# Kernel optimization log

Measured on AMD Instinct MI355X. Metric: run time of the kernel, lower is better.

The kernel has to match this reference:

```python
import jax, jax.numpy as jnp
import numpy as np


def setup_inputs() -> dict:
    key = jax.random.key(0)
    k1, k2, *kw = jax.random.split(key, 12)
    N, E = 10000, 320000
    D_IN, D_HID, D_EMB, D_PRED = 2, 128, 256, 128

    def lin(k, fan_in, fan_out):
        bound = 1.0 / np.sqrt(fan_in)
        kw_, kb_ = jax.random.split(k)
        W = jax.random.uniform(kw_, (fan_in, fan_out), jnp.float32, -bound, bound)
        b = jax.random.uniform(kb_, (fan_out,), jnp.float32, -bound, bound)
        return W, b

    W1, b1 = lin(kw[0], D_IN, D_HID)
    W2, b2 = lin(kw[1], D_HID, D_EMB)
    Wp1, bp1 = lin(kw[2], D_EMB, D_PRED)
    Wp2, bp2 = lin(kw[3], D_PRED, 1)

    src = jax.random.randint(k1, (E,), 0, N, dtype=jnp.int32)
    dst = jax.random.randint(k2, (E,), 0, N, dtype=jnp.int32)
    return {
        "W1": W1, "b1": b1, "W2": W2, "b2": b2,
        "Wp1": Wp1, "bp1": bp1, "Wp2": Wp2, "bp2": bp2,
        "src": src, "dst": dst, "num_nodes": N,
    }


def reference(W1, b1, W2, b2, Wp1, bp1, Wp2, bp2, src, dst, num_nodes):
    N = num_nodes
    E = src.shape[0]
    ones = jnp.ones((E,), jnp.float32)
    # node features = [in_degree, out_degree]  -> [N, 2]
    in_deg = jax.ops.segment_sum(ones, dst, num_segments=N)
    out_deg = jax.ops.segment_sum(ones, src, num_segments=N)
    x = jnp.stack([in_deg, out_deg], axis=1)

    def gcn_agg(h):
        # sum of messages from source nodes into destination nodes (SpMM-like)
        return jax.ops.segment_sum(h[src], dst, num_segments=N)

    h = jax.nn.relu(gcn_agg(x) @ W1 + b1)        # [N, 128]
    h = gcn_agg(h) @ W2 + b2                     # [N, 256]
    h = jax.nn.relu(h)
    graph_embedding = jnp.sum(h, axis=0)         # [256] (dgl.sum_nodes, single graph)
    m = jax.nn.relu(graph_embedding @ Wp1 + bp1)
    metric = m @ Wp2 + bp2                       # [1]
    return (graph_embedding, metric)
```

## Files before the change

kernel.cpp:

```cpp
#include <hip/hip_runtime.h>

#define N_NODES 10000
#define CAPLOG 7
#define CAP 128
#define NPART 16
#define NBH 128
#define TBH 512

__global__ __launch_bounds__(TBH) void hist_kernel(const int* __restrict__ src,
                                                   const int* __restrict__ dst,
                                                   unsigned int* __restrict__ cnt, int E) {
  __shared__ unsigned int hist[N_NODES];
  const int tid = threadIdx.x, bid = blockIdx.x;
  for (int i = tid; i < N_NODES; i += TBH) hist[i] = 0;
  __syncthreads();
  const int chunk = (E + NBH - 1) / NBH;
  const int e0 = bid * chunk, e1 = min(E, e0 + chunk);
  for (int e = e0 + tid; e < e1; e += TBH) {
    atomicAdd(&hist[dst[e]], 1u);
    atomicAdd(&hist[src[e]], 0x10000u);
  }
  __syncthreads();
  unsigned int* outb = cnt + (size_t)bid * N_NODES;
  for (int i = tid; i < N_NODES; i += TBH) outb[i] = hist[i];
}

__global__ __launch_bounds__(256) void scan_kernel(const unsigned int* __restrict__ cnt,
                                                   unsigned int* __restrict__ off,
                                                   unsigned int* __restrict__ pack) {
  const int n = blockIdx.x * 256 + threadIdx.x;
  if (n >= N_NODES) return;
  unsigned run_in = 0, run_out = 0;
  for (int b = 0; b < NBH; ++b) {
    unsigned v = cnt[(size_t)b * N_NODES + n];
    off[(size_t)b * N_NODES + n] = run_in;
    run_in += v & 0xFFFFu;
    run_out += v >> 16;
  }
  pack[n] = run_in | (run_out << 16);
}

__global__ __launch_bounds__(TBH) void scatter_kernel(const int* __restrict__ src,
                                                      const int* __restrict__ dst,
                                                      const unsigned int* __restrict__ off,
                                                      unsigned short* __restrict__ slots,
                                                      int E) {
  __shared__ unsigned int cur[N_NODES];
  const int tid = threadIdx.x, bid = blockIdx.x;
  const unsigned int* ob = off + (size_t)bid * N_NODES;
  for (int i = tid; i < N_NODES; i += TBH) cur[i] = ob[i];
  __syncthreads();
  const int chunk = (E + NBH - 1) / NBH;
  const int e0 = bid * chunk, e1 = min(E, e0 + chunk);
  for (int e = e0 + tid; e < e1; e += TBH) {
    int d = dst[e];
    unsigned idx = atomicAdd(&cur[d], 1u);
    if (idx < CAP) slots[(d << CAPLOG) + idx] = (unsigned short)src[e];
  }
}

__global__ __launch_bounds__(256) void agg1_kernel(const unsigned int* __restrict__ pack,
                                                   const unsigned short* __restrict__ slots,
                                                   float2* __restrict__ a) {
  const int tid = threadIdx.x;
  const int hw = tid >> 5, hl = tid & 31;
  const int node = blockIdx.x * 8 + hw;
  const int deg = min((int)(pack[node] & 0xFFFFu), CAP);
  const int base = node << CAPLOG;
  float a0 = 0.f, a1 = 0.f;
  for (int e = hl; e < deg; e += 32) {
    unsigned v = pack[slots[base + e]];
    a0 += (float)(v & 0xFFFFu);
    a1 += (float)(v >> 16);
  }
#pragma unroll
  for (int off = 16; off > 0; off >>= 1) {
    a0 += __shfl_xor(a0, off);
    a1 += __shfl_xor(a1, off);
  }
  if (hl == 0) a[node] = make_float2(a0, a1);
}

__global__ __launch_bounds__(256) void agg2gemm2_kernel(const unsigned int* __restrict__ pack,
                                                        const unsigned short* __restrict__ slots,
                                                        const float2* __restrict__ a,
                                                        const float* __restrict__ W1,
                                                        const float* __restrict__ b1,
                                                        const float* __restrict__ W2,
                                                        const float* __restrict__ b2,
                                                        float* __restrict__ ge_p) {
  __shared__ float s_tile[8][128];
  const int tid = threadIdx.x, bid = blockIdx.x;
  const int hw = tid >> 5, hl = tid & 31;

  float w10[4], w11[4], bb[4];
#pragma unroll
  for (int c = 0; c < 4; ++c) {
    w10[c] = W1[4 * hl + c];
    w11[c] = W1[128 + 4 * hl + c];
    bb[c] = b1[4 * hl + c];
  }
  const int node = bid * 8 + hw;
  const int deg = min((int)(pack[node] & 0xFFFFu), CAP);
  float acc0 = 0.f, acc1 = 0.f, acc2 = 0.f, acc3 = 0.f;
  int rem = deg, eb = node << CAPLOG;
  while (rem > 0) {
    int cnt = min(rem, 32);
    float va0 = 0.f, va1 = 0.f;
    if (hl < cnt) {
      float2 av = a[slots[eb + hl]];
      va0 = av.x;
      va1 = av.y;
    }
    for (int j = 0; j < cnt; ++j) {
      float x0 = __shfl(va0, j, 32);
      float x1 = __shfl(va1, j, 32);
      acc0 += fmaxf(fmaf(x0, w10[0], fmaf(x1, w11[0], bb[0])), 0.f);
      acc1 += fmaxf(fmaf(x0, w10[1], fmaf(x1, w11[1], bb[1])), 0.f);
      acc2 += fmaxf(fmaf(x0, w10[2], fmaf(x1, w11[2], bb[2])), 0.f);
      acc3 += fmaxf(fmaf(x0, w10[3], fmaf(x1, w11[3], bb[3])), 0.f);
    }
    rem -= cnt;
    eb += cnt;
  }
  s_tile[hw][4 * hl + 0] = acc0;
  s_tile[hw][4 * hl + 1] = acc1;
  s_tile[hw][4 * hl + 2] = acc2;
  s_tile[hw][4 * hl + 3] = acc3;
  __syncthreads();

  float d[8];
#pragma unroll
  for (int n = 0; n < 8; ++n) d[n] = 0.f;
#pragma unroll
  for (int kc = 0; kc < 4; ++kc) {
    float wv[32];
#pragma unroll
    for (int c = 0; c < 32; ++c) wv[c] = W2[(kc * 32 + c) * 256 + tid];
#pragma unroll
    for (int n = 0; n < 8; ++n) {
      const float4* row4 = (const float4*)&s_tile[n][kc * 32];
      float t0 = 0.f, t1 = 0.f, t2 = 0.f, t3 = 0.f;
#pragma unroll
      for (int q = 0; q < 8; ++q) {
        float4 rv = row4[q];
        t0 = fmaf(rv.x, wv[4 * q + 0], t0);
        t1 = fmaf(rv.y, wv[4 * q + 1], t1);
        t2 = fmaf(rv.z, wv[4 * q + 2], t2);
        t3 = fmaf(rv.w, wv[4 * q + 3], t3);
      }
      d[n] += (t0 + t1) + (t2 + t3);
    }
  }

  const float bj = b2[tid];
  float accge = 0.f;
#pragma unroll
  for (int n = 0; n < 8; ++n) accge += fmaxf(d[n] + bj, 0.f);
  atomicAdd(&ge_p[((bid & (NPART - 1)) << 8) + tid], accge);
}

__global__ __launch_bounds__(256) void head_kernel(const float* __restrict__ ge_p,
                                                   const float* __restrict__ Wp1,
                                                   const float* __restrict__ bp1,
                                                   const float* __restrict__ Wp2,
                                                   const float* __restrict__ bp2,
                                                   float* __restrict__ out) {
  __shared__ float s_ge[256];
  __shared__ float s_m[256];
  int tid = threadIdx.x;
  float g = 0.f;
#pragma unroll
  for (int p = 0; p < NPART; ++p) g += ge_p[p * 256 + tid];
  s_ge[tid] = g;
  out[tid] = g;
  __syncthreads();
  int j = tid & 127, halfk = tid >> 7;
  float d = halfk ? 0.f : bp1[j];
  int k0 = halfk << 7;
#pragma unroll 8
  for (int k = k0; k < k0 + 128; ++k) d = fmaf(s_ge[k], Wp1[k * 128 + j], d);
  s_m[tid] = d;
  __syncthreads();
  if (tid < 128) s_m[tid] = fmaxf(s_m[tid] + s_m[tid + 128], 0.f) * Wp2[tid];
  __syncthreads();
  if (tid < 64) {
    float v = s_m[tid] + s_m[tid + 64];
#pragma unroll
    for (int off = 32; off > 0; off >>= 1) v += __shfl_xor(v, off);
    if (tid == 0) out[256] = v + bp2[0];
  }
}

extern "C" void kernel_launch(void* const* d_in, const int* in_sizes, int n_in,
                              void* d_out, int out_size, void* d_ws, size_t ws_size,
                              hipStream_t stream) {
  const float* W1 = (const float*)d_in[0];
  const float* b1 = (const float*)d_in[1];
  const float* W2 = (const float*)d_in[2];
  const float* b2 = (const float*)d_in[3];
  const float* Wp1 = (const float*)d_in[4];
  const float* bp1 = (const float*)d_in[5];
  const float* Wp2 = (const float*)d_in[6];
  const float* bp2 = (const float*)d_in[7];
  const int* src = (const int*)d_in[8];
  const int* dst = (const int*)d_in[9];
  const int E = in_sizes[8];
  const int N = N_NODES;

  char* p = (char*)d_ws;
  float* ge_p = (float*)p;               p += (size_t)NPART * 256 * 4;
  unsigned int* pack = (unsigned int*)p; p += (size_t)N * 4;
  unsigned short* slots = (unsigned short*)p; p += (size_t)N * CAP * 2;
  float2* a = (float2*)p;                p += (size_t)N * 8;
  unsigned int* cnt = (unsigned int*)p;  p += (size_t)NBH * N * 4;
  unsigned int* off = (unsigned int*)p;
  float* out = (float*)d_out;

  hipMemsetAsync(d_ws, 0, (size_t)NPART * 256 * 4, stream);

  hist_kernel<<<NBH, TBH, 0, stream>>>(src, dst, cnt, E);
  scan_kernel<<<(N + 255) / 256, 256, 0, stream>>>(cnt, off, pack);
  scatter_kernel<<<NBH, TBH, 0, stream>>>(src, dst, off, slots, E);
  agg1_kernel<<<N / 8, 256, 0, stream>>>(pack, slots, a);
  agg2gemm2_kernel<<<N / 8, 256, 0, stream>>>(pack, slots, a, W1, b1, W2, b2, ge_p);
  head_kernel<<<1, 256, 0, stream>>>(ge_p, Wp1, bp1, Wp2, bp2, out);
}
```

Before: 135.0 us.

## Replace histogram-scan-scatter CSR build with per-node-range full-edge scan and fuse head

Replaces the three-kernel histogram, scan and scatter CSR construction with a prep kernel that packs src/dst into 32-bit edge words, followed by a build kernel. In the build kernel, each block scans every edge and keeps only those whose destination or source falls in its 40-node range. The first aggregation now stores packed integer degree sums instead of float2, halving the gather traffic. The head MLP is fused into the last block of the GEMM kernel through a done counter, and the memset is folded into the prep kernel. The cost is that each of the 250 blocks rereads the whole edge list, trading redundant L2 reads for fewer launches and no large count and offset arrays. Slot order within a node becomes nondeterministic, which changes float summation order.

```diff
diff --git a/kernel.cpp b/kernel.cpp
--- a/kernel.cpp
+++ b/kernel.cpp
@@ -4,92 +4,120 @@
 #define CAPLOG 7
 #define CAP 128
 #define NPART 16
-#define NBH 128
-#define TBH 512
-
-__global__ __launch_bounds__(TBH) void hist_kernel(const int* __restrict__ src,
-                                                   const int* __restrict__ dst,
-                                                   unsigned int* __restrict__ cnt, int E) {
-  __shared__ unsigned int hist[N_NODES];
-  const int tid = threadIdx.x, bid = blockIdx.x;
-  for (int i = tid; i < N_NODES; i += TBH) hist[i] = 0;
-  __syncthreads();
-  const int chunk = (E + NBH - 1) / NBH;
-  const int e0 = bid * chunk, e1 = min(E, e0 + chunk);
-  for (int e = e0 + tid; e < e1; e += TBH) {
-    atomicAdd(&hist[dst[e]], 1u);
-    atomicAdd(&hist[src[e]], 0x10000u);
-  }
-  __syncthreads();
-  unsigned int* outb = cnt + (size_t)bid * N_NODES;
-  for (int i = tid; i < N_NODES; i += TBH) outb[i] = hist[i];
-}
-
-__global__ __launch_bounds__(256) void scan_kernel(const unsigned int* __restrict__ cnt,
-                                                   unsigned int* __restrict__ off,
-                                                   unsigned int* __restrict__ pack) {
-  const int n = blockIdx.x * 256 + threadIdx.x;
-  if (n >= N_NODES) return;
-  unsigned run_in = 0, run_out = 0;
-  for (int b = 0; b < NBH; ++b) {
-    unsigned v = cnt[(size_t)b * N_NODES + n];
-    off[(size_t)b * N_NODES + n] = run_in;
-    run_in += v & 0xFFFFu;
-    run_out += v >> 16;
-  }
-  pack[n] = run_in | (run_out << 16);
-}
-
-__global__ __launch_bounds__(TBH) void scatter_kernel(const int* __restrict__ src,
+
+#define NBB 250
+#define TBB 1024
+#define NPB 40
+
+#define PREP_T 256
+__global__ __launch_bounds__(PREP_T) void prep_kernel(const int* __restrict__ src,
                                                       const int* __restrict__ dst,
-                                                      const unsigned int* __restrict__ off,
-                                                      unsigned short* __restrict__ slots,
+                                                      unsigned int* __restrict__ ed,
+                                                      float* __restrict__ ge_p,
+                                                      unsigned int* __restrict__ done,
                                                       int E) {
-  __shared__ unsigned int cur[N_NODES];
-  const int tid = threadIdx.x, bid = blockIdx.x;
-  const unsigned int* ob = off + (size_t)bid * N_NODES;
-  for (int i = tid; i < N_NODES; i += TBH) cur[i] = ob[i];
-  __syncthreads();
-  const int chunk = (E + NBH - 1) / NBH;
-  const int e0 = bid * chunk, e1 = min(E, e0 + chunk);
-  for (int e = e0 + tid; e < e1; e += TBH) {
-    int d = dst[e];
-    unsigned idx = atomicAdd(&cur[d], 1u);
-    if (idx < CAP) slots[(d << CAPLOG) + idx] = (unsigned short)src[e];
-  }
+  const int t = blockIdx.x * PREP_T + threadIdx.x;
+  if (t < NPART * 256) ge_p[t] = 0.f;
+  if (t == NPART * 256) *done = 0u;
+  const int nv = E >> 3;
+  if (t < nv) {
+    const int4* s4 = (const int4*)src;
+    const int4* d4 = (const int4*)dst;
+    int4 s0 = s4[2 * t], s1 = s4[2 * t + 1];
+    int4 d0 = d4[2 * t], d1 = d4[2 * t + 1];
+    uint4 o0, o1;
+    o0.x = (unsigned)d0.x | ((unsigned)s0.x << 16);
+    o0.y = (unsigned)d0.y | ((unsigned)s0.y << 16);
+    o0.z = (unsigned)d0.z | ((unsigned)s0.z << 16);
+    o0.w = (unsigned)d0.w | ((unsigned)s0.w << 16);
+    o1.x = (unsigned)d1.x | ((unsigned)s1.x << 16);
+    o1.y = (unsigned)d1.y | ((unsigned)s1.y << 16);
+    o1.z = (unsigned)d1.z | ((unsigned)s1.z << 16);
+    o1.w = (unsigned)d1.w | ((unsigned)s1.w << 16);
+    ((uint4*)ed)[2 * t + 0] = o0;
+    ((uint4*)ed)[2 * t + 1] = o1;
+  }
+  if (t == 0) {
+    for (int e = E & ~7; e < E; ++e)
+      ed[e] = ((unsigned)dst[e] & 0xFFFFu) | ((unsigned)src[e] << 16);
+  }
+}
+
+__global__ __launch_bounds__(TBB) void build_kernel(const unsigned int* __restrict__ ed,
+                                                    unsigned short* __restrict__ slots,
+                                                    unsigned int* __restrict__ pack,
+                                                    int E) {
+  __shared__ unsigned int cin[NPB], cout[NPB];
+  const int tid = threadIdx.x;
+  const unsigned n0 = blockIdx.x * NPB;
+  if (tid < NPB) { cin[tid] = 0u; cout[tid] = 0u; }
+  __syncthreads();
+  const int nv = E >> 2;
+  const uint4* e4 = (const uint4*)ed;
+  for (int c = tid; c < nv; c += TBB) {
+    uint4 v = e4[c];
+    unsigned w[4] = {v.x, v.y, v.z, v.w};
+#pragma unroll
+    for (int q = 0; q < 4; ++q) {
+      const unsigned d = w[q] & 0xFFFFu, s = w[q] >> 16;
+      const unsigned rd = d - n0;
+      if (rd < NPB) {
+        unsigned idx = atomicAdd(&cin[rd], 1u);
+        if (idx < CAP) slots[(d << CAPLOG) + idx] = (unsigned short)s;
+      }
+      const unsigned rs = s - n0;
+      if (rs < NPB) atomicAdd(&cout[rs], 1u);
+    }
+  }
+  if (tid == 0) {
+    for (int e = E & ~3; e < E; ++e) {
+      const unsigned d = ed[e] & 0xFFFFu, s = ed[e] >> 16;
+      const unsigned rd = d - n0;
+      if (rd < NPB) {
+        unsigned idx = atomicAdd(&cin[rd], 1u);
+        if (idx < CAP) slots[(d << CAPLOG) + idx] = (unsigned short)s;
+      }
+      const unsigned rs = s - n0;
+      if (rs < NPB) atomicAdd(&cout[rs], 1u);
+    }
+  }
+  __syncthreads();
+  if (tid < NPB) pack[n0 + tid] = cin[tid] | (cout[tid] << 16);
 }
 
 __global__ __launch_bounds__(256) void agg1_kernel(const unsigned int* __restrict__ pack,
                                                    const unsigned short* __restrict__ slots,
-                                                   float2* __restrict__ a) {
+                                                   unsigned int* __restrict__ a) {
   const int tid = threadIdx.x;
   const int hw = tid >> 5, hl = tid & 31;
   const int node = blockIdx.x * 8 + hw;
   const int deg = min((int)(pack[node] & 0xFFFFu), CAP);
   const int base = node << CAPLOG;
-  float a0 = 0.f, a1 = 0.f;
-  for (int e = hl; e < deg; e += 32) {
-    unsigned v = pack[slots[base + e]];
-    a0 += (float)(v & 0xFFFFu);
-    a1 += (float)(v >> 16);
-  }
-#pragma unroll
-  for (int off = 16; off > 0; off >>= 1) {
-    a0 += __shfl_xor(a0, off);
-    a1 += __shfl_xor(a1, off);
-  }
-  if (hl == 0) a[node] = make_float2(a0, a1);
+  unsigned acc = 0u;
+  for (int e = hl; e < deg; e += 32) acc += pack[slots[base + e]];
+#pragma unroll
+  for (int off = 16; off > 0; off >>= 1) acc += (unsigned)__shfl_xor((int)acc, off);
+  if (hl == 0) a[node] = acc;
 }
 
 __global__ __launch_bounds__(256) void agg2gemm2_kernel(const unsigned int* __restrict__ pack,
                                                         const unsigned short* __restrict__ slots,
-                                                        const float2* __restrict__ a,
+                                                        const unsigned int* __restrict__ a,
                                                         const float* __restrict__ W1,
                                                         const float* __restrict__ b1,
                                                         const float* __restrict__ W2,
                                                         const float* __restrict__ b2,
-                                                        float* __restrict__ ge_p) {
+                                                        const float* __restrict__ Wp1,
+                                                        const float* __restrict__ bp1,
+                                                        const float* __restrict__ Wp2,
+                                                        const float* __restrict__ bp2,
+                                                        float* __restrict__ ge_p,
+                                                        unsigned int* __restrict__ done,
+                                                        float* __restrict__ out) {
   __shared__ float s_tile[8][128];
+  __shared__ float s_ge[256];
+  __shared__ float s_m[256];
+  __shared__ int s_last;
   const int tid = threadIdx.x, bid = blockIdx.x;
   const int hw = tid >> 5, hl = tid & 31;
 
@@ -106,15 +134,12 @@
   int rem = deg, eb = node << CAPLOG;
   while (rem > 0) {
     int cnt = min(rem, 32);
-    float va0 = 0.f, va1 = 0.f;
-    if (hl < cnt) {
-      float2 av = a[slots[eb + hl]];
-      va0 = av.x;
-      va1 = av.y;
-    }
+    unsigned av = 0u;
+    if (hl < cnt) av = a[slots[eb + hl]];
     for (int j = 0; j < cnt; ++j) {
-      float x0 = __shfl(va0, j, 32);
-      float x1 = __shfl(va1, j, 32);
+      const unsigned v = (unsigned)__shfl((int)av, j, 32);
+      const float x0 = (float)(v & 0xFFFFu);
+      const float x1 = (float)(v >> 16);
       acc0 += fmaxf(fmaf(x0, w10[0], fmaf(x1, w11[0], bb[0])), 0.f);
       acc1 += fmaxf(fmaf(x0, w10[1], fmaf(x1, w11[1], bb[1])), 0.f);
       acc2 += fmaxf(fmaf(x0, w10[2], fmaf(x1, w11[2], bb[2])), 0.f);
@@ -158,29 +183,28 @@
 #pragma unroll
   for (int n = 0; n < 8; ++n) accge += fmaxf(d[n] + bj, 0.f);
   atomicAdd(&ge_p[((bid & (NPART - 1)) << 8) + tid], accge);
-}
-
-__global__ __launch_bounds__(256) void head_kernel(const float* __restrict__ ge_p,
-                                                   const float* __restrict__ Wp1,
-                                                   const float* __restrict__ bp1,
-                                                   const float* __restrict__ Wp2,
-                                                   const float* __restrict__ bp2,
-                                                   float* __restrict__ out) {
-  __shared__ float s_ge[256];
-  __shared__ float s_m[256];
-  int tid = threadIdx.x;
+
+  __syncthreads();
+  if (tid == 0) {
+    __threadfence();
+    s_last = (atomicAdd(done, 1u) == (unsigned)(gridDim.x - 1)) ? 1 : 0;
+  }
+  __syncthreads();
+  if (!s_last) return;
+
   float g = 0.f;
 #pragma unroll
-  for (int p = 0; p < NPART; ++p) g += ge_p[p * 256 + tid];
+  for (int p = 0; p < NPART; ++p)
+    g += __hip_atomic_load(&ge_p[p * 256 + tid], __ATOMIC_RELAXED, __HIP_MEMORY_SCOPE_AGENT);
   s_ge[tid] = g;
   out[tid] = g;
   __syncthreads();
-  int j = tid & 127, halfk = tid >> 7;
-  float d = halfk ? 0.f : bp1[j];
-  int k0 = halfk << 7;
+  const int j = tid & 127, halfk = tid >> 7;
+  float dd = halfk ? 0.f : bp1[j];
+  const int k0 = halfk << 7;
 #pragma unroll 8
-  for (int k = k0; k < k0 + 128; ++k) d = fmaf(s_ge[k], Wp1[k * 128 + j], d);
-  s_m[tid] = d;
+  for (int k = k0; k < k0 + 128; ++k) dd = fmaf(s_ge[k], Wp1[k * 128 + j], dd);
+  s_m[tid] = dd;
   __syncthreads();
   if (tid < 128) s_m[tid] = fmaxf(s_m[tid] + s_m[tid + 128], 0.f) * Wp2[tid];
   __syncthreads();
@@ -210,19 +234,18 @@
 
   char* p = (char*)d_ws;
   float* ge_p = (float*)p;               p += (size_t)NPART * 256 * 4;
+  unsigned int* done = (unsigned int*)p; p += 16;
   unsigned int* pack = (unsigned int*)p; p += (size_t)N * 4;
+  unsigned int* a = (unsigned int*)p;    p += (size_t)N * 4;
   unsigned short* slots = (unsigned short*)p; p += (size_t)N * CAP * 2;
-  float2* a = (float2*)p;                p += (size_t)N * 8;
-  unsigned int* cnt = (unsigned int*)p;  p += (size_t)NBH * N * 4;
-  unsigned int* off = (unsigned int*)p;
+  unsigned int* ed = (unsigned int*)p;
   float* out = (float*)d_out;
 
-  hipMemsetAsync(d_ws, 0, (size_t)NPART * 256 * 4, stream);
-
-  hist_kernel<<<NBH, TBH, 0, stream>>>(src, dst, cnt, E);
-  scan_kernel<<<(N + 255) / 256, 256, 0, stream>>>(cnt, off, pack);
-  scatter_kernel<<<NBH, TBH, 0, stream>>>(src, dst, off, slots, E);
+  const int nv8 = (E + 7) / 8;
+  const int prep_threads = (nv8 > NPART * 256 + 1) ? nv8 : (NPART * 256 + 1);
+  prep_kernel<<<(prep_threads + PREP_T - 1) / PREP_T, PREP_T, 0, stream>>>(src, dst, ed, ge_p, done, E);
+  build_kernel<<<NBB, TBB, 0, stream>>>(ed, slots, pack, E);
   agg1_kernel<<<N / 8, 256, 0, stream>>>(pack, slots, a);
-  agg2gemm2_kernel<<<N / 8, 256, 0, stream>>>(pack, slots, a, W1, b1, W2, b2, ge_p);
-  head_kernel<<<1, 256, 0, stream>>>(ge_p, Wp1, bp1, Wp2, bp2, out);
-}
+  agg2gemm2_kernel<<<N / 8, 256, 0, stream>>>(pack, slots, a, W1, b1, W2, b2,
+                                              Wp1, bp1, Wp2, bp2, ge_p, done, out);
+}
```

Result: slower. 166.0 us (+23.0%).

## Materialize layer-1 activations, gather rows in agg2, fuse head via last-block

Applied to the files above, without the earlier changes.

Moves the first linear+ReLU into agg1, which now writes a full [N,128] hidden matrix. agg2 then gathers and sums neighbor rows with wide loads instead of recomputing relu(W1·x) per edge through shuffles. The memset and head kernel launches are removed: hist zeroes the partial sums and a done counter, and the last block of agg2 computes the head after a threadfence and atomic ticket. The scan also sums the packed in/out counts as one word. In exchange, agg2 does more gather traffic (about 5 MB of h written and reread per edge), and the packed 16-bit in/out counters become fragile if a node's degree carries past 16 bits.

```diff
diff --git a/kernel.cpp b/kernel.cpp
--- a/kernel.cpp
+++ b/kernel.cpp
@@ -9,10 +9,15 @@
 
 __global__ __launch_bounds__(TBH) void hist_kernel(const int* __restrict__ src,
                                                    const int* __restrict__ dst,
-                                                   unsigned int* __restrict__ cnt, int E) {
+                                                   unsigned int* __restrict__ cnt,
+                                                   float* __restrict__ ge_p,
+                                                   unsigned int* __restrict__ done,
+                                                   int E) {
   __shared__ unsigned int hist[N_NODES];
   const int tid = threadIdx.x, bid = blockIdx.x;
   for (int i = tid; i < N_NODES; i += TBH) hist[i] = 0;
+  if (bid < NPART && tid < 256) ge_p[(bid << 8) + tid] = 0.f;
+  if (bid == NPART && tid == 0) *done = 0u;
   __syncthreads();
   const int chunk = (E + NBH - 1) / NBH;
   const int e0 = bid * chunk, e1 = min(E, e0 + chunk);
@@ -30,14 +35,14 @@
                                                    unsigned int* __restrict__ pack) {
   const int n = blockIdx.x * 256 + threadIdx.x;
   if (n >= N_NODES) return;
-  unsigned run_in = 0, run_out = 0;
+  unsigned run = 0;
+#pragma unroll 8
   for (int b = 0; b < NBH; ++b) {
     unsigned v = cnt[(size_t)b * N_NODES + n];
-    off[(size_t)b * N_NODES + n] = run_in;
-    run_in += v & 0xFFFFu;
-    run_out += v >> 16;
-  }
-  pack[n] = run_in | (run_out << 16);
+    off[(size_t)b * N_NODES + n] = run;
+    run += v;
+  }
+  pack[n] = run;
 }
 
 __global__ __launch_bounds__(TBH) void scatter_kernel(const int* __restrict__ src,
@@ -54,79 +59,77 @@
   const int e0 = bid * chunk, e1 = min(E, e0 + chunk);
   for (int e = e0 + tid; e < e1; e += TBH) {
     int d = dst[e];
-    unsigned idx = atomicAdd(&cur[d], 1u);
+    unsigned idx = atomicAdd(&cur[d], 1u) & 0xFFFFu;
     if (idx < CAP) slots[(d << CAPLOG) + idx] = (unsigned short)src[e];
   }
 }
 
-__global__ __launch_bounds__(256) void agg1_kernel(const unsigned int* __restrict__ pack,
-                                                   const unsigned short* __restrict__ slots,
-                                                   float2* __restrict__ a) {
+__global__ __launch_bounds__(256) void agg1h_kernel(const unsigned int* __restrict__ pack,
+                                                    const unsigned short* __restrict__ slots,
+                                                    const float* __restrict__ W1,
+                                                    const float* __restrict__ b1,
+                                                    float* __restrict__ h) {
   const int tid = threadIdx.x;
   const int hw = tid >> 5, hl = tid & 31;
   const int node = blockIdx.x * 8 + hw;
   const int deg = min((int)(pack[node] & 0xFFFFu), CAP);
   const int base = node << CAPLOG;
-  float a0 = 0.f, a1 = 0.f;
-  for (int e = hl; e < deg; e += 32) {
-    unsigned v = pack[slots[base + e]];
-    a0 += (float)(v & 0xFFFFu);
-    a1 += (float)(v >> 16);
-  }
-#pragma unroll
-  for (int off = 16; off > 0; off >>= 1) {
-    a0 += __shfl_xor(a0, off);
-    a1 += __shfl_xor(a1, off);
-  }
-  if (hl == 0) a[node] = make_float2(a0, a1);
+  unsigned acc = 0u;
+  for (int e = hl; e < deg; e += 32) acc += pack[slots[base + e]];
+#pragma unroll
+  for (int off = 16; off > 0; off >>= 1) acc += (unsigned)__shfl_xor((int)acc, off, 32);
+  const float a0 = (float)(acc & 0xFFFFu);
+  const float a1 = (float)(acc >> 16);
+  const int c = 4 * hl;
+  float4 hv;
+  hv.x = fmaxf(fmaf(a0, W1[c + 0], fmaf(a1, W1[128 + c + 0], b1[c + 0])), 0.f);
+  hv.y = fmaxf(fmaf(a0, W1[c + 1], fmaf(a1, W1[128 + c + 1], b1[c + 1])), 0.f);
+  hv.z = fmaxf(fmaf(a0, W1[c + 2], fmaf(a1, W1[128 + c + 2], b1[c + 2])), 0.f);
+  hv.w = fmaxf(fmaf(a0, W1[c + 3], fmaf(a1, W1[128 + c + 3], b1[c + 3])), 0.f);
+  ((float4*)h)[node * 32 + hl] = hv;
 }
 
 __global__ __launch_bounds__(256) void agg2gemm2_kernel(const unsigned int* __restrict__ pack,
                                                         const unsigned short* __restrict__ slots,
-                                                        const float2* __restrict__ a,
-                                                        const float* __restrict__ W1,
-                                                        const float* __restrict__ b1,
+                                                        const float* __restrict__ h,
                                                         const float* __restrict__ W2,
                                                         const float* __restrict__ b2,
-                                                        float* __restrict__ ge_p) {
+                                                        const float* __restrict__ Wp1,
+                                                        const float* __restrict__ bp1,
+                                                        const float* __restrict__ Wp2,
+                                                        const float* __restrict__ bp2,
+                                                        float* __restrict__ ge_p,
+                                                        unsigned int* __restrict__ done,
+                                                        float* __restrict__ out) {
   __shared__ float s_tile[8][128];
+  __shared__ float s_ge[256];
+  __shared__ float s_m[256];
+  __shared__ int s_last;
   const int tid = threadIdx.x, bid = blockIdx.x;
-  const int hw = tid >> 5, hl = tid & 31;
-
-  float w10[4], w11[4], bb[4];
-#pragma unroll
-  for (int c = 0; c < 4; ++c) {
-    w10[c] = W1[4 * hl + c];
-    w11[c] = W1[128 + 4 * hl + c];
-    bb[c] = b1[4 * hl + c];
-  }
-  const int node = bid * 8 + hw;
-  const int deg = min((int)(pack[node] & 0xFFFFu), CAP);
-  float acc0 = 0.f, acc1 = 0.f, acc2 = 0.f, acc3 = 0.f;
-  int rem = deg, eb = node << CAPLOG;
-  while (rem > 0) {
-    int cnt = min(rem, 32);
-    float va0 = 0.f, va1 = 0.f;
-    if (hl < cnt) {
-      float2 av = a[slots[eb + hl]];
-      va0 = av.x;
-      va1 = av.y;
+  const int wv = tid >> 6, lane = tid & 63;
+  const float2* h2 = (const float2*)h;
+
+#pragma unroll
+  for (int nn = 0; nn < 2; ++nn) {
+    const int node = bid * 8 + 2 * wv + nn;
+    const int deg = min((int)(pack[node] & 0xFFFFu), CAP);
+    const unsigned* sl32 = (const unsigned*)(slots + (node << CAPLOG));
+    float2 acc = make_float2(0.f, 0.f);
+    for (int i0 = 0; i0 < deg; i0 += 8) {
+      const uint4 sw = ((const uint4*)sl32)[i0 >> 3];
+      const unsigned ss[4] = {sw.x, sw.y, sw.z, sw.w};
+#pragma unroll
+      for (int q = 0; q < 8; ++q) {
+        if (i0 + q < deg) {
+          const int s = (q & 1) ? (int)(ss[q >> 1] >> 16) : (int)(ss[q >> 1] & 0xFFFFu);
+          const float2 v = h2[s * 64 + lane];
+          acc.x += v.x;
+          acc.y += v.y;
+        }
+      }
     }
-    for (int j = 0; j < cnt; ++j) {
-      float x0 = __shfl(va0, j, 32);
-      float x1 = __shfl(va1, j, 32);
-      acc0 += fmaxf(fmaf(x0, w10[0], fmaf(x1, w11[0], bb[0])), 0.f);
-      acc1 += fmaxf(fmaf(x0, w10[1], fmaf(x1, w11[1], bb[1])), 0.f);
-      acc2 += fmaxf(fmaf(x0, w10[2], fmaf(x1, w11[2], bb[2])), 0.f);
-      acc3 += fmaxf(fmaf(x0, w10[3], fmaf(x1, w11[3], bb[3])), 0.f);
-    }
-    rem -= cnt;
-    eb += cnt;
-  }
-  s_tile[hw][4 * hl + 0] = acc0;
-  s_tile[hw][4 * hl + 1] = acc1;
-  s_tile[hw][4 * hl + 2] = acc2;
-  s_tile[hw][4 * hl + 3] = acc3;
+    ((float2*)&s_tile[2 * wv + nn][0])[lane] = acc;
+  }
   __syncthreads();
 
   float d[8];
@@ -134,9 +137,9 @@
   for (int n = 0; n < 8; ++n) d[n] = 0.f;
 #pragma unroll
   for (int kc = 0; kc < 4; ++kc) {
-    float wv[32];
-#pragma unroll
-    for (int c = 0; c < 32; ++c) wv[c] = W2[(kc * 32 + c) * 256 + tid];
+    float wvv[32];
+#pragma unroll
+    for (int c = 0; c < 32; ++c) wvv[c] = W2[(kc * 32 + c) * 256 + tid];
 #pragma unroll
     for (int n = 0; n < 8; ++n) {
       const float4* row4 = (const float4*)&s_tile[n][kc * 32];
@@ -144,10 +147,10 @@
 #pragma unroll
       for (int q = 0; q < 8; ++q) {
         float4 rv = row4[q];
-        t0 = fmaf(rv.x, wv[4 * q + 0], t0);
-        t1 = fmaf(rv.y, wv[4 * q + 1], t1);
-        t2 = fmaf(rv.z, wv[4 * q + 2], t2);
-        t3 = fmaf(rv.w, wv[4 * q + 3], t3);
+        t0 = fmaf(rv.x, wvv[4 * q + 0], t0);
+        t1 = fmaf(rv.y, wvv[4 * q + 1], t1);
+        t2 = fmaf(rv.z, wvv[4 * q + 2], t2);
+        t3 = fmaf(rv.w, wvv[4 * q + 3], t3);
       }
       d[n] += (t0 + t1) + (t2 + t3);
     }
@@ -158,29 +161,28 @@
 #pragma unroll
   for (int n = 0; n < 8; ++n) accge += fmaxf(d[n] + bj, 0.f);
   atomicAdd(&ge_p[((bid & (NPART - 1)) << 8) + tid], accge);
-}
-
-__global__ __launch_bounds__(256) void head_kernel(const float* __restrict__ ge_p,
-                                                   const float* __restrict__ Wp1,
-                                                   const float* __restrict__ bp1,
-                                                   const float* __restrict__ Wp2,
-                                                   const float* __restrict__ bp2,
-                                                   float* __restrict__ out) {
-  __shared__ float s_ge[256];
-  __shared__ float s_m[256];
-  int tid = threadIdx.x;
+
+  __syncthreads();
+  if (tid == 0) {
+    __threadfence();
+    s_last = (atomicAdd(done, 1u) == (unsigned)(gridDim.x - 1)) ? 1 : 0;
+  }
+  __syncthreads();
+  if (!s_last) return;
+
   float g = 0.f;
 #pragma unroll
-  for (int p = 0; p < NPART; ++p) g += ge_p[p * 256 + tid];
+  for (int p = 0; p < NPART; ++p)
+    g += __hip_atomic_load(&ge_p[p * 256 + tid], __ATOMIC_RELAXED, __HIP_MEMORY_SCOPE_AGENT);
   s_ge[tid] = g;
   out[tid] = g;
   __syncthreads();
-  int j = tid & 127, halfk = tid >> 7;
-  float d = halfk ? 0.f : bp1[j];
-  int k0 = halfk << 7;
+  const int j = tid & 127, halfk = tid >> 7;
+  float dd = halfk ? 0.f : bp1[j];
+  const int k0 = halfk << 7;
 #pragma unroll 8
-  for (int k = k0; k < k0 + 128; ++k) d = fmaf(s_ge[k], Wp1[k * 128 + j], d);
-  s_m[tid] = d;
+  for (int k = k0; k < k0 + 128; ++k) dd = fmaf(s_ge[k], Wp1[k * 128 + j], dd);
+  s_m[tid] = dd;
   __syncthreads();
   if (tid < 128) s_m[tid] = fmaxf(s_m[tid] + s_m[tid + 128], 0.f) * Wp2[tid];
   __syncthreads();
@@ -210,19 +212,18 @@
 
   char* p = (char*)d_ws;
   float* ge_p = (float*)p;               p += (size_t)NPART * 256 * 4;
+  unsigned int* done = (unsigned int*)p; p += 16;
   unsigned int* pack = (unsigned int*)p; p += (size_t)N * 4;
   unsigned short* slots = (unsigned short*)p; p += (size_t)N * CAP * 2;
-  float2* a = (float2*)p;                p += (size_t)N * 8;
+  float* h = (float*)p;                  p += (size_t)N * 128 * 4;
   unsigned int* cnt = (unsigned int*)p;  p += (size_t)NBH * N * 4;
   unsigned int* off = (unsigned int*)p;
   float* out = (float*)d_out;
 
-  hipMemsetAsync(d_ws, 0, (size_t)NPART * 256 * 4, stream);
-
-  hist_kernel<<<NBH, TBH, 0, stream>>>(src, dst, cnt, E);
+  hist_kernel<<<NBH, TBH, 0, stream>>>(src, dst, cnt, ge_p, done, E);
   scan_kernel<<<(N + 255) / 256, 256, 0, stream>>>(cnt, off, pack);
   scatter_kernel<<<NBH, TBH, 0, stream>>>(src, dst, off, slots, E);
-  agg1_kernel<<<N / 8, 256, 0, stream>>>(pack, slots, a);
-  agg2gemm2_kernel<<<N / 8, 256, 0, stream>>>(pack, slots, a, W1, b1, W2, b2, ge_p);
-  head_kernel<<<1, 256, 0, stream>>>(ge_p, Wp1, bp1, Wp2, bp2, out);
-}
+  agg1h_kernel<<<N / 8, 256, 0, stream>>>(pack, slots, W1, b1, h);
+  agg2gemm2_kernel<<<N / 8, 256, 0, stream>>>(pack, slots, h, W2, b2,
+                                              Wp1, bp1, Wp2, bp2, ge_p, done, out);
+}
```

New measurement: 165.3 us. 1.22x slower.
